# Optimization experiments

Measured on AMD Instinct MI355X. Metric: run time of the kernel, lower is better.

## Reference

```python
import jax, jax.numpy as jnp
import numpy as np
from jax import lax

B, S, IN, H, HEAD, OUT = 256, 512, 64, 1024, 128, 64


def setup_inputs() -> dict:
    key = jax.random.key(0)
    ks = jax.random.split(key, 9)
    sc = 0.05
    return {
        "x": jax.random.normal(ks[0], (B, S, IN), jnp.float32),
        "W_ih": jax.random.normal(ks[1], (4 * H, IN), jnp.float32) * sc,
        "b_ih": jax.random.normal(ks[2], (4 * H,), jnp.float32) * sc,
        "W_hh": jax.random.normal(ks[3], (4 * H, H), jnp.float32) * sc,
        "b_hh": jax.random.normal(ks[4], (4 * H,), jnp.float32) * sc,
        "W_dense": jax.random.normal(ks[5], (HEAD, H), jnp.float32) * sc,
        "b_dense": jax.random.normal(ks[6], (HEAD,), jnp.float32) * sc,
        "W_dense2": jax.random.normal(ks[7], (OUT, HEAD), jnp.float32) * sc,
        "b_dense2": jax.random.normal(ks[8], (OUT,), jnp.float32) * sc,
    }


def reference(x, W_ih, b_ih, W_hh, b_hh, W_dense, b_dense, W_dense2, b_dense2):
    batch = x.shape[0]
    hid = W_hh.shape[1]
    # Precompute input-to-gate projections for all timesteps in one big GEMM.
    # x: [B,S,IN] -> xg: [S,B,4H]
    xg = jnp.einsum("bsi,gi->sbg", x, W_ih) + b_ih + b_hh

    def step(carry, xg_t):
        h, c = carry
        gates = xg_t + h @ W_hh.T  # [B,4H]; PyTorch LSTMCell gate order i,f,g,o
        i, f, g, o = jnp.split(gates, 4, axis=-1)
        c = jax.nn.sigmoid(f) * c + jax.nn.sigmoid(i) * jnp.tanh(g)
        h = jax.nn.sigmoid(o) * jnp.tanh(c)
        pred = jax.nn.relu(h @ W_dense.T + b_dense) @ W_dense2.T + b_dense2
        return (h, c), pred

    h0 = jnp.zeros((batch, hid), x.dtype)
    c0 = jnp.zeros((batch, hid), x.dtype)
    _, out = lax.scan(step, (h0, c0), xg)  # out: [S,B,OUT]
    return jnp.swapaxes(out, 0, 1)  # [B,S,OUT]
```

## Files before the change

### kernel.cpp

```cpp
#include <hip/hip_runtime.h>

typedef _Float16 half_t;
typedef _Float16 half8 __attribute__((ext_vector_type(8)));
typedef _Float16 half4 __attribute__((ext_vector_type(4)));
typedef float float4v __attribute__((ext_vector_type(4)));

#define BB    256
#define SS    512
#define IND   64
#define HH    1024
#define HEADD 128
#define OUTD  64
#define NKT   34
#define WLDS_HALVES (4 * NKT * 512)
#define PRE_STRIDE 68
#define DP_OFF   (WLDS_HALVES * 2 + 4 * 16 * PRE_STRIDE * 4)
#define FLAG_OFF (DP_OFF + 3 * 64 * 4 * 4)
#define SMEM_BYTES (FLAG_OFF + 32)
#define BUFV (BB * HH)
#define GO_OFF   8192
#define DCNT_OFF 10240
#define SYNC_WORDS 10368

#define MFMA16(a, b, acc) __builtin_amdgcn_mfma_f32_16x16x32_f16(a, b, acc, 0, 0, 0)

__device__ half_t g_hA[(size_t)(SS + 1) * BUFV];
__device__ half_t g_dbuf[(size_t)SS * 256 * HEADD];
__device__ unsigned int g_sync[SYNC_WORDS];

__device__ __forceinline__ void astore8(half_t* p, half4 v) {
  union { half4 h; unsigned long long u; } r; r.h = v;
  __hip_atomic_store((unsigned long long*)p, r.u, __ATOMIC_RELAXED,
                     __HIP_MEMORY_SCOPE_AGENT);
}
__device__ __forceinline__ void astore2(half_t* p, half_t v) {
  union { half_t h; unsigned short u; } r; r.h = v;
  __hip_atomic_store((unsigned short*)p, r.u, __ATOMIC_RELAXED,
                     __HIP_MEMORY_SCOPE_AGENT);
}


__global__ __launch_bounds__(256) void init_state() {
  const size_t i = (size_t)blockIdx.x * 256 + threadIdx.x;
  *(unsigned long long*)(g_hA + i * 4) = 0ULL;
  if (blockIdx.x == 0)
    for (int j = threadIdx.x; j < SYNC_WORDS; j += 256) g_sync[j] = 0;
}

__global__ __launch_bounds__(256) void pack_x(const float* __restrict__ x,
                                              half_t* __restrict__ xA) {
  const int t = blockIdx.x, mt = blockIdx.y;
  const int tid = threadIdx.x;
  const int kt = tid >> 7;
  const int lane = (tid >> 1) & 63;
  const int jh = (tid & 1) * 4;
  const int row = mt * 16 + (lane & 15);
  const int k = kt * 32 + (lane >> 4) * 8 + jh;
  const float* s = x + (size_t)row * SS * IND + (size_t)t * IND + k;
  half_t* d = xA + (((size_t)t * 16 + mt) * 2 + kt) * 512 + lane * 8 + jh;
  d[0] = (half_t)s[0]; d[1] = (half_t)s[1];
  d[2] = (half_t)s[2]; d[3] = (half_t)s[3];
}

__global__ __launch_bounds__(256) void frag_pack(const float* __restrict__ src,
                                                 half_t* __restrict__ dst, int K) {
  const int cb = blockIdx.x;
  const int tid = threadIdx.x;
  const int lane = tid & 63;
  const int u = tid >> 6;
  const int nkt = K >> 5;
  const int row = cb * 16 + (lane & 15);
  for (int kt = u; kt < nkt; kt += 4) {
    const int k = kt * 32 + (lane >> 4) * 8;
    const float* s = src + (size_t)row * K + k;
    half8 h;
    #pragma unroll
    for (int j = 0; j < 8; ++j) h[j] = (half_t)s[j];
    *(half8*)(dst + ((size_t)cb * nkt + kt) * 512 + lane * 8) = h;
  }
}

__global__ __launch_bounds__(512, 2) void lstm_persistent(
    const float* __restrict__ W_hh, const float* __restrict__ W_ih,
    const float* __restrict__ b_ih, const float* __restrict__ b_hh,
    const half_t* __restrict__ xA, const half_t* __restrict__ Wd_f,
    const float* __restrict__ bd, const half_t* __restrict__ Wd2_f,
    const float* __restrict__ bd2, float* __restrict__ out) {
  extern __shared__ char smem[];
  half_t* Wlds = (half_t*)smem;
  float* pre = (float*)(smem + (size_t)WLDS_HALVES * 2);
  float* dp = (float*)(smem + DP_OFF);
  unsigned* flg = (unsigned*)(smem + FLAG_OFF);

  const int wg = blockIdx.x;
  const int mtile = wg >> 6;
  const int jtile = wg & 63;
  const int j0 = jtile * 16;
  const int tid = threadIdx.x;
  const int wave = tid >> 6;
  const int lane = tid & 63;
  const int rn = lane & 15;
  const int kq = lane >> 4;

  {
    const int g = wave & 3;
    const int row = g * HH + j0 + rn;
    for (int kt = (wave >> 2); kt < NKT; kt += 2) {
      const int k = kt * 32 + kq * 8;
      const float* s = (k < HH) ? (W_hh + (size_t)row * HH + k)
                                : (W_ih + (size_t)row * IND + (k - HH));
      half8 hv;
      #pragma unroll
      for (int j = 0; j < 8; ++j) hv[j] = (half_t)s[j];
      *(half8*)(Wlds + ((size_t)g * NKT + kt) * 512 + lane * 8) = hv;
    }
  }
  if (tid < 8) flg[tid] = 0;
  __syncthreads();

  unsigned short* slotp =
      (unsigned short*)(g_sync + ((size_t)(mtile * 64 + jtile)) * 32);
  unsigned int* go_base = g_sync + GO_OFF + mtile * 512;
  const unsigned int* gop = go_base + (jtile & 15) * 32;
  unsigned int* dcnt = g_sync + DCNT_OFF + mtile * 32;

  if (wave < 4) {
    const int crow = lane >> 2;
    const int hl = (lane & 3) * 4;
    float bsum[4][4];
    #pragma unroll
    for (int g = 0; g < 4; ++g) {
      const float4v bi = *(const float4v*)(b_ih + g * HH + j0 + hl);
      const float4v bh = *(const float4v*)(b_hh + g * HH + j0 + hl);
      #pragma unroll
      for (int j = 0; j < 4; ++j) bsum[g][j] = bi[j] + bh[j];
    }
    float4v creg = {0.f, 0.f, 0.f, 0.f};

    const int mtA = mtile * 4 + wave;
    float* pw = pre + wave * (16 * PRE_STRIDE);

    const int col_s = j0 + hl;
    const int ktw = col_s >> 5;
    const int kqw = (col_s & 31) >> 3;
    const int jw = col_s & 7;
    const size_t hoff =
        (((size_t)(mtA * 32 + ktw)) * 64 + kqw * 16 + crow) * 8 + jw;

    const half_t* habase = g_hA + ((size_t)mtA * 32) * 512 + lane * 8;
    const half_t* bp = Wlds + lane * 8;
    unsigned short* myslot = slotp + wave;

    for (int t = 0; t < SS; ++t) {
      float4v a0 = {0.f, 0.f, 0.f, 0.f}, a1 = {0.f, 0.f, 0.f, 0.f};
      float4v a2 = {0.f, 0.f, 0.f, 0.f}, a3 = {0.f, 0.f, 0.f, 0.f};

      const half_t* xp = xA + (((size_t)t * 16 + mtA) * 2) * 512 + lane * 8;
      {
        const half8 xv0 = *(const half8*)xp;
        const half8 xv1 = *(const half8*)(xp + 512);
        a0 = MFMA16(xv0, *(const half8*)(bp + (size_t)(0 * NKT + 32) * 512), a0);
        a1 = MFMA16(xv0, *(const half8*)(bp + (size_t)(1 * NKT + 32) * 512), a1);
        a2 = MFMA16(xv0, *(const half8*)(bp + (size_t)(2 * NKT + 32) * 512), a2);
        a3 = MFMA16(xv0, *(const half8*)(bp + (size_t)(3 * NKT + 32) * 512), a3);
        a0 = MFMA16(xv1, *(const half8*)(bp + (size_t)(0 * NKT + 33) * 512), a0);
        a1 = MFMA16(xv1, *(const half8*)(bp + (size_t)(1 * NKT + 33) * 512), a1);
        a2 = MFMA16(xv1, *(const half8*)(bp + (size_t)(2 * NKT + 33) * 512), a2);
        a3 = MFMA16(xv1, *(const half8*)(bp + (size_t)(3 * NKT + 33) * 512), a3);
      }

      if (t >= 1) {
        const unsigned tt = (unsigned)t;
        while (__hip_atomic_load(gop, __ATOMIC_RELAXED,
                                 __HIP_MEMORY_SCOPE_AGENT) < tt)
          __builtin_amdgcn_s_sleep(2);
        asm volatile("" ::: "memory");
        if (wave == 0 && lane == 0)
          __hip_atomic_store(&flg[3], tt, __ATOMIC_RELEASE,
                             __HIP_MEMORY_SCOPE_WORKGROUP);
      }

      const half_t* ap = habase + (size_t)t * BUFV;
      #pragma unroll 8
      for (int kt = 0; kt < 32; ++kt) {
        const half8 av = *(const half8*)(ap + (size_t)kt * 512);
        a0 = MFMA16(av, *(const half8*)(bp + (size_t)(0 * NKT + kt) * 512), a0);
        a1 = MFMA16(av, *(const half8*)(bp + (size_t)(1 * NKT + kt) * 512), a1);
        a2 = MFMA16(av, *(const half8*)(bp + (size_t)(2 * NKT + kt) * 512), a2);
        a3 = MFMA16(av, *(const half8*)(bp + (size_t)(3 * NKT + kt) * 512), a3);
      }

      #pragma unroll
      for (int r = 0; r < 4; ++r) {
        const int rl = (kq * 4 + r) * PRE_STRIDE;
        pw[rl + rn] = a0[r];
        pw[rl + 16 + rn] = a1[r];
        pw[rl + 32 + rn] = a2[r];
        pw[rl + 48 + rn] = a3[r];
      }

      const float4v pg0 = *(const float4v*)(pw + crow * PRE_STRIDE + hl);
      const float4v pg1 = *(const float4v*)(pw + crow * PRE_STRIDE + 16 + hl);
      const float4v pg2 = *(const float4v*)(pw + crow * PRE_STRIDE + 32 + hl);
      const float4v pg3 = *(const float4v*)(pw + crow * PRE_STRIDE + 48 + hl);
      half4 hnew;
      #pragma unroll
      for (int jj = 0; jj < 4; ++jj) {
        const float ig = pg0[jj] + bsum[0][jj];
        const float fg = pg1[jj] + bsum[1][jj];
        const float gg = pg2[jj] + bsum[2][jj];
        const float og = pg3[jj] + bsum[3][jj];
        const float is = 1.f / (1.f + __expf(-ig));
        const float fs = 1.f / (1.f + __expf(-fg));
        const float os = 1.f / (1.f + __expf(-og));
        const float gt = tanhf(gg);
        const float cn = fs * creg[jj] + is * gt;
        creg[jj] = cn;
        hnew[jj] = (half_t)(os * tanhf(cn));
      }
      astore8(g_hA + (size_t)(t + 1) * BUFV + hoff, hnew);

      __builtin_amdgcn_s_waitcnt(0);
      if (lane == 0)
        __hip_atomic_store(myslot, (unsigned short)(t + 1), __ATOMIC_RELAXED,
                           __HIP_MEMORY_SCOPE_AGENT);
    }

    if (wave == 0) {
      while (__hip_atomic_load(gop, __ATOMIC_RELAXED,
                               __HIP_MEMORY_SCOPE_AGENT) < (unsigned)SS)
        __builtin_amdgcn_s_sleep(2);
      asm volatile("" ::: "memory");
      if (lane == 0)
        __hip_atomic_store(&flg[3], (unsigned)SS, __ATOMIC_RELEASE,
                           __HIP_MEMORY_SCOPE_WORKGROUP);
    }

  } else if (jtile < 32) {
    const int u = wave - 4;
    const int rb = jtile >> 3, cb = jtile & 7;
    const int mt = mtile * 4 + rb;
    const half_t* hb = g_hA + ((size_t)mt * 32 + u * 8) * 512 + lane * 8;
    const half_t* bb = Wd_f + ((size_t)cb * 32 + u * 8) * 512 + lane * 8;

    for (int s = 1; s <= SS; ++s) {
      while (__hip_atomic_load(&flg[3], __ATOMIC_ACQUIRE,
                               __HIP_MEMORY_SCOPE_WORKGROUP) < (unsigned)s)
        __builtin_amdgcn_s_sleep(2);
      asm volatile("" ::: "memory");

      const half_t* ap = hb + (size_t)s * BUFV;
      float4v acc = {0.f, 0.f, 0.f, 0.f};
      #pragma unroll
      for (int kt = 0; kt < 8; ++kt)
        acc = MFMA16(*(const half8*)(ap + (size_t)kt * 512),
                     *(const half8*)(bb + (size_t)kt * 512), acc);

      if (u) {
        if (s > 1)
          while (__hip_atomic_load(&flg[4], __ATOMIC_ACQUIRE,
                                   __HIP_MEMORY_SCOPE_WORKGROUP) <
                 (unsigned)(s - 1))
            __builtin_amdgcn_s_sleep(1);
        *(float4v*)(dp + ((size_t)(u - 1) * 64 + lane) * 4) = acc;
        __hip_atomic_store(&flg[u - 1], (unsigned)s, __ATOMIC_RELEASE,
                           __HIP_MEMORY_SCOPE_WORKGROUP);
      } else {
        for (;;) {
          const unsigned f0 = __hip_atomic_load(&flg[0], __ATOMIC_ACQUIRE,
                                                __HIP_MEMORY_SCOPE_WORKGROUP);
          const unsigned f1 = __hip_atomic_load(&flg[1], __ATOMIC_ACQUIRE,
                                                __HIP_MEMORY_SCOPE_WORKGROUP);
          const unsigned f2 = __hip_atomic_load(&flg[2], __ATOMIC_ACQUIRE,
                                                __HIP_MEMORY_SCOPE_WORKGROUP);
          if (f0 >= (unsigned)s && f1 >= (unsigned)s && f2 >= (unsigned)s) break;
          __builtin_amdgcn_s_sleep(1);
        }
        asm volatile("" ::: "memory");
        #pragma unroll
        for (int i = 0; i < 3; ++i) {
          const float4v p = *(const float4v*)(dp + ((size_t)i * 64 + lane) * 4);
          #pragma unroll
          for (int r = 0; r < 4; ++r) acc[r] += p[r];
        }
        __hip_atomic_store(&flg[4], (unsigned)s, __ATOMIC_RELEASE,
                           __HIP_MEMORY_SCOPE_WORKGROUP);
        const int dcol = cb * 16 + rn;
        const float bv = bd[dcol];
        half_t* db = g_dbuf + (((size_t)(s - 1) * 16 + mt) * 16) * HEADD + dcol;
        #pragma unroll
        for (int r = 0; r < 4; ++r)
          astore2(db + (size_t)(kq * 4 + r) * HEADD,
                  (half_t)fmaxf(acc[r] + bv, 0.f));
        __builtin_amdgcn_s_waitcnt(0);
        if (lane == 0)
          __hip_atomic_fetch_add(dcnt, 1u, __ATOMIC_RELAXED,
                                 __HIP_MEMORY_SCOPE_AGENT);
      }
    }

  } else if (jtile < 48 && wave == 4) {
    const int task = jtile - 32;
    const int rb = task >> 2, cb2 = task & 3;
    const int mt = mtile * 4 + rb;
    const int m0 = mtile * 64;
    const half_t* bp2 = Wd2_f + (size_t)cb2 * 4 * 512 + lane * 8;
    for (int d = 0; d < SS; ++d) {
      if (lane == 0) {
        const unsigned tgt = 32u * (unsigned)(d + 1);
        while (__hip_atomic_load(dcnt, __ATOMIC_RELAXED,
                                 __HIP_MEMORY_SCOPE_AGENT) < tgt)
          __builtin_amdgcn_s_sleep(16);
      }
      asm volatile("" ::: "memory");
      const half_t* ap = g_dbuf + (((size_t)d * 16 + mt) * 16) * HEADD;
      float4v acc = {0.f, 0.f, 0.f, 0.f};
      #pragma unroll
      for (int kt = 0; kt < 4; ++kt) {
        const half8 af =
            *(const half8*)(ap + (size_t)rn * HEADD + kt * 32 + kq * 8);
        acc = MFMA16(af, *(const half8*)(bp2 + (size_t)kt * 512), acc);
      }
      const int ocol = cb2 * 16 + rn;
      const float bv = bd2[ocol];
      #pragma unroll
      for (int r = 0; r < 4; ++r) {
        const int row = m0 + rb * 16 + kq * 4 + r;
        out[(size_t)row * (SS * OUTD) + (size_t)d * OUTD + ocol] = acc[r] + bv;
      }
    }

  } else if (jtile == 63 && wave == 5) {
    const unsigned long long* pollp =
        (const unsigned long long*)(g_sync + ((size_t)(mtile * 64 + lane)) * 32);
    for (int t = 1; t <= SS; ++t) {
      const unsigned tt = (unsigned)t;
      for (;;) {
        const unsigned long long v = __hip_atomic_load(
            pollp, __ATOMIC_RELAXED, __HIP_MEMORY_SCOPE_AGENT);
        const unsigned f0 = (unsigned)(v & 0xffffu);
        const unsigned f1 = (unsigned)((v >> 16) & 0xffffu);
        const unsigned f2 = (unsigned)((v >> 32) & 0xffffu);
        const unsigned f3 = (unsigned)(v >> 48);
        if (__all((int)(f0 >= tt && f1 >= tt && f2 >= tt && f3 >= tt))) break;
        __builtin_amdgcn_s_sleep(2);
      }
      asm volatile("" ::: "memory");
      if (lane < 16)
        __hip_atomic_store(go_base + lane * 32, tt, __ATOMIC_RELAXED,
                           __HIP_MEMORY_SCOPE_AGENT);
    }
  }
}

extern "C" void kernel_launch(void* const* d_in, const int* in_sizes, int n_in,
                              void* d_out, int out_size, void* d_ws, size_t ws_size,
                              hipStream_t stream) {
  const float* x        = (const float*)d_in[0];
  const float* W_ih     = (const float*)d_in[1];
  const float* b_ih     = (const float*)d_in[2];
  const float* W_hh     = (const float*)d_in[3];
  const float* b_hh     = (const float*)d_in[4];
  const float* W_dense  = (const float*)d_in[5];
  const float* b_dense  = (const float*)d_in[6];
  const float* W_dense2 = (const float*)d_in[7];
  const float* b_dense2 = (const float*)d_in[8];
  float* out = (float*)d_out;

  char* p = (char*)d_ws;
  half_t* xA    = (half_t*)p; p += (size_t)SS * 16 * 1024 * 2;
  half_t* Wd_f  = (half_t*)p; p += (size_t)8 * 32 * 512 * 2;
  half_t* Wd2_f = (half_t*)p; p += (size_t)4 * 4 * 512 * 2;

  init_state<<<256, 256, 0, stream>>>();
  pack_x<<<dim3(SS, 16), 256, 0, stream>>>(x, xA);
  frag_pack<<<HEADD / 16, 256, 0, stream>>>(W_dense, Wd_f, HH);
  frag_pack<<<OUTD / 16, 256, 0, stream>>>(W_dense2, Wd2_f, HEADD);

  hipFuncSetAttribute((const void*)lstm_persistent,
                      hipFuncAttributeMaxDynamicSharedMemorySize, SMEM_BYTES);
  void* args[] = {(void*)&W_hh, (void*)&W_ih, (void*)&b_ih, (void*)&b_hh,
                  (void*)&xA, (void*)&Wd_f, (void*)&b_dense,
                  (void*)&Wd2_f, (void*)&b_dense2, (void*)&out};
  hipLaunchCooperativeKernel((void*)lstm_persistent, dim3(256), dim3(512),
                             args, SMEM_BYTES, stream);
}
```

Before: 4.797 ms.

## Replace aggregator-wave barrier with per-chunk atomic counters and staged K-waits

Drops the dedicated aggregator wave that polled every workgroup's slot flags and broadcast a go counter. Each workgroup now counts its four waves' completion in LDS and the last wave increments one of four global per-timestep chunk counters. The recurrent GEMM is split into four K-chunks, and each chunk waits only on the counter for the producers of that slice, so MFMA work can start before all of h_t is ready. This removes one hop of barrier latency from the serial timestep chain, at the cost of more global atomic contention and more polling loads.

```diff
diff --git a/kernel.cpp b/kernel.cpp
--- a/kernel.cpp
+++ b/kernel.cpp
@@ -16,11 +16,10 @@
 #define PRE_STRIDE 68
 #define DP_OFF   (WLDS_HALVES * 2 + 4 * 16 * PRE_STRIDE * 4)
 #define FLAG_OFF (DP_OFF + 3 * 64 * 4 * 4)
-#define SMEM_BYTES (FLAG_OFF + 32)
+#define SMEM_BYTES (FLAG_OFF + 96)
 #define BUFV (BB * HH)
-#define GO_OFF   8192
-#define DCNT_OFF 10240
-#define SYNC_WORDS 10368
+#define DCNT_OFF 8192
+#define SYNC_WORDS 8320
 
 #define MFMA16(a, b, acc) __builtin_amdgcn_mfma_f32_16x16x32_f16(a, b, acc, 0, 0, 0)
 
@@ -91,6 +90,7 @@
   float* pre = (float*)(smem + (size_t)WLDS_HALVES * 2);
   float* dp = (float*)(smem + DP_OFF);
   unsigned* flg = (unsigned*)(smem + FLAG_OFF);
+  unsigned* wgdone = flg + 8;
 
   const int wg = blockIdx.x;
   const int mtile = wg >> 6;
@@ -116,12 +116,10 @@
     }
   }
   if (tid < 8) flg[tid] = 0;
+  if (tid >= 8 && tid < 24) wgdone[tid - 8] = 0;
   __syncthreads();
 
-  unsigned short* slotp =
-      (unsigned short*)(g_sync + ((size_t)(mtile * 64 + jtile)) * 32);
-  unsigned int* go_base = g_sync + GO_OFF + mtile * 512;
-  const unsigned int* gop = go_base + (jtile & 15) * 32;
+  unsigned int* cbase = g_sync + (size_t)mtile * 2048;
   unsigned int* dcnt = g_sync + DCNT_OFF + mtile * 32;
 
   if (wave < 4) {
@@ -149,9 +147,21 @@
 
     const half_t* habase = g_hA + ((size_t)mtA * 32) * 512 + lane * 8;
     const half_t* bp = Wlds + lane * 8;
-    unsigned short* myslot = slotp + wave;
+    const int mychunk = jtile >> 4;
 
     for (int t = 0; t < SS; ++t) {
+      unsigned r0 = 16u, r1 = 16u, r2 = 16u, r3 = 16u;
+      if (t >= 1) {
+        r0 = __hip_atomic_load(cbase + 0 * 512 + (t - 1), __ATOMIC_RELAXED,
+                               __HIP_MEMORY_SCOPE_AGENT);
+        r1 = __hip_atomic_load(cbase + 1 * 512 + (t - 1), __ATOMIC_RELAXED,
+                               __HIP_MEMORY_SCOPE_AGENT);
+        r2 = __hip_atomic_load(cbase + 2 * 512 + (t - 1), __ATOMIC_RELAXED,
+                               __HIP_MEMORY_SCOPE_AGENT);
+        r3 = __hip_atomic_load(cbase + 3 * 512 + (t - 1), __ATOMIC_RELAXED,
+                               __HIP_MEMORY_SCOPE_AGENT);
+      }
+
       float4v a0 = {0.f, 0.f, 0.f, 0.f}, a1 = {0.f, 0.f, 0.f, 0.f};
       float4v a2 = {0.f, 0.f, 0.f, 0.f}, a3 = {0.f, 0.f, 0.f, 0.f};
 
@@ -169,25 +179,30 @@
         a3 = MFMA16(xv1, *(const half8*)(bp + (size_t)(3 * NKT + 33) * 512), a3);
       }
 
-      if (t >= 1) {
-        const unsigned tt = (unsigned)t;
-        while (__hip_atomic_load(gop, __ATOMIC_RELAXED,
-                                 __HIP_MEMORY_SCOPE_AGENT) < tt)
-          __builtin_amdgcn_s_sleep(2);
-        asm volatile("" ::: "memory");
-        if (wave == 0 && lane == 0)
-          __hip_atomic_store(&flg[3], tt, __ATOMIC_RELEASE,
-                             __HIP_MEMORY_SCOPE_WORKGROUP);
-      }
-
       const half_t* ap = habase + (size_t)t * BUFV;
-      #pragma unroll 8
-      for (int kt = 0; kt < 32; ++kt) {
-        const half8 av = *(const half8*)(ap + (size_t)kt * 512);
-        a0 = MFMA16(av, *(const half8*)(bp + (size_t)(0 * NKT + kt) * 512), a0);
-        a1 = MFMA16(av, *(const half8*)(bp + (size_t)(1 * NKT + kt) * 512), a1);
-        a2 = MFMA16(av, *(const half8*)(bp + (size_t)(2 * NKT + kt) * 512), a2);
-        a3 = MFMA16(av, *(const half8*)(bp + (size_t)(3 * NKT + kt) * 512), a3);
+      #pragma unroll
+      for (int q = 0; q < 4; ++q) {
+        if (t >= 1) {
+          unsigned v = (q == 0) ? r0 : (q == 1) ? r1 : (q == 2) ? r2 : r3;
+          while (v < 16u) {
+            __builtin_amdgcn_s_sleep(1);
+            v = __hip_atomic_load(cbase + q * 512 + (t - 1), __ATOMIC_RELAXED,
+                                  __HIP_MEMORY_SCOPE_AGENT);
+          }
+          asm volatile("" ::: "memory");
+          if (q == 3 && wave == 0 && lane == 0)
+            __hip_atomic_store(&flg[3], (unsigned)t, __ATOMIC_RELEASE,
+                               __HIP_MEMORY_SCOPE_WORKGROUP);
+        }
+        #pragma unroll
+        for (int k2 = 0; k2 < 8; ++k2) {
+          const int kt = q * 8 + k2;
+          const half8 av = *(const half8*)(ap + (size_t)kt * 512);
+          a0 = MFMA16(av, *(const half8*)(bp + (size_t)(0 * NKT + kt) * 512), a0);
+          a1 = MFMA16(av, *(const half8*)(bp + (size_t)(1 * NKT + kt) * 512), a1);
+          a2 = MFMA16(av, *(const half8*)(bp + (size_t)(2 * NKT + kt) * 512), a2);
+          a3 = MFMA16(av, *(const half8*)(bp + (size_t)(3 * NKT + kt) * 512), a3);
+        }
       }
 
       #pragma unroll
@@ -221,15 +236,24 @@
       astore8(g_hA + (size_t)(t + 1) * BUFV + hoff, hnew);
 
       __builtin_amdgcn_s_waitcnt(0);
-      if (lane == 0)
-        __hip_atomic_store(myslot, (unsigned short)(t + 1), __ATOMIC_RELAXED,
-                           __HIP_MEMORY_SCOPE_AGENT);
+      asm volatile("" ::: "memory");
+      if (lane == 0) {
+        const unsigned old = atomicAdd(&wgdone[t & 15], 1u);
+        if (old == 3u) {
+          wgdone[t & 15] = 0u;
+          __hip_atomic_fetch_add(cbase + mychunk * 512 + t, 1u,
+                                 __ATOMIC_RELAXED, __HIP_MEMORY_SCOPE_AGENT);
+        }
+      }
     }
 
     if (wave == 0) {
-      while (__hip_atomic_load(gop, __ATOMIC_RELAXED,
-                               __HIP_MEMORY_SCOPE_AGENT) < (unsigned)SS)
-        __builtin_amdgcn_s_sleep(2);
+      #pragma unroll
+      for (int q = 0; q < 4; ++q) {
+        while (__hip_atomic_load(cbase + q * 512 + (SS - 1), __ATOMIC_RELAXED,
+                                 __HIP_MEMORY_SCOPE_AGENT) < 16u)
+          __builtin_amdgcn_s_sleep(2);
+      }
       asm volatile("" ::: "memory");
       if (lane == 0)
         __hip_atomic_store(&flg[3], (unsigned)SS, __ATOMIC_RELEASE,
@@ -329,27 +353,6 @@
         out[(size_t)row * (SS * OUTD) + (size_t)d * OUTD + ocol] = acc[r] + bv;
       }
     }
-
-  } else if (jtile == 63 && wave == 5) {
-    const unsigned long long* pollp =
-        (const unsigned long long*)(g_sync + ((size_t)(mtile * 64 + lane)) * 32);
-    for (int t = 1; t <= SS; ++t) {
-      const unsigned tt = (unsigned)t;
-      for (;;) {
-        const unsigned long long v = __hip_atomic_load(
-            pollp, __ATOMIC_RELAXED, __HIP_MEMORY_SCOPE_AGENT);
-        const unsigned f0 = (unsigned)(v & 0xffffu);
-        const unsigned f1 = (unsigned)((v >> 16) & 0xffffu);
-        const unsigned f2 = (unsigned)((v >> 32) & 0xffffu);
-        const unsigned f3 = (unsigned)(v >> 48);
-        if (__all((int)(f0 >= tt && f1 >= tt && f2 >= tt && f3 >= tt))) break;
-        __builtin_amdgcn_s_sleep(2);
-      }
-      asm volatile("" ::: "memory");
-      if (lane < 16)
-        __hip_atomic_store(go_base + lane * 32, tt, __ATOMIC_RELAXED,
-                           __HIP_MEMORY_SCOPE_AGENT);
-    }
   }
 }
 
```

Measured after the change: 5.884 ms. +22.6%, slower.

## Split step barrier into per-quarter go flags so GEMM starts on partial h

Applied to the files above, without the earlier changes.

The coordinator wave now reduces completion slots per group of 16 workgroups and publishes four separate go counters (one per K-quarter of h) rather than a single all-done flag. Gate-compute waves begin the recurrent GEMM as soon as the first quarter is ready and wait for each later quarter just before its K-slice. Dense-head waves poll their own quarter's go flag directly instead of the workgroup-local relay flag. The aim is to overlap the global step barrier with MFMA work, at the cost of more polling traffic and a more complex, fragile synchronization protocol.

```diff
diff --git a/kernel.cpp b/kernel.cpp
--- a/kernel.cpp
+++ b/kernel.cpp
@@ -80,6 +80,15 @@
   }
 }
 
+#define GKT(kt)                                                               \
+  {                                                                           \
+    const half8 av = *(const half8*)(ap + (size_t)(kt) * 512);                \
+    a0 = MFMA16(av, *(const half8*)(bp + (size_t)(0 * NKT + (kt)) * 512), a0);\
+    a1 = MFMA16(av, *(const half8*)(bp + (size_t)(1 * NKT + (kt)) * 512), a1);\
+    a2 = MFMA16(av, *(const half8*)(bp + (size_t)(2 * NKT + (kt)) * 512), a2);\
+    a3 = MFMA16(av, *(const half8*)(bp + (size_t)(3 * NKT + (kt)) * 512), a3);\
+  }
+
 __global__ __launch_bounds__(512, 2) void lstm_persistent(
     const float* __restrict__ W_hh, const float* __restrict__ W_ih,
     const float* __restrict__ b_ih, const float* __restrict__ b_hh,
@@ -121,7 +130,7 @@
   unsigned short* slotp =
       (unsigned short*)(g_sync + ((size_t)(mtile * 64 + jtile)) * 32);
   unsigned int* go_base = g_sync + GO_OFF + mtile * 512;
-  const unsigned int* gop = go_base + (jtile & 15) * 32;
+  const unsigned int* goline = go_base + (jtile & 15) * 32;
   unsigned int* dcnt = g_sync + DCNT_OFF + mtile * 32;
 
   if (wave < 4) {
@@ -152,6 +161,18 @@
     unsigned short* myslot = slotp + wave;
 
     for (int t = 0; t < SS; ++t) {
+      unsigned g0 = 0, g1 = 0, g2 = 0, g3 = 0;
+      if (t >= 1) {
+        const unsigned long long v01 = __hip_atomic_load(
+            (const unsigned long long*)goline, __ATOMIC_RELAXED,
+            __HIP_MEMORY_SCOPE_AGENT);
+        const unsigned long long v23 = __hip_atomic_load(
+            (const unsigned long long*)(goline + 2), __ATOMIC_RELAXED,
+            __HIP_MEMORY_SCOPE_AGENT);
+        g0 = (unsigned)v01; g1 = (unsigned)(v01 >> 32);
+        g2 = (unsigned)v23; g3 = (unsigned)(v23 >> 32);
+      }
+
       float4v a0 = {0.f, 0.f, 0.f, 0.f}, a1 = {0.f, 0.f, 0.f, 0.f};
       float4v a2 = {0.f, 0.f, 0.f, 0.f}, a3 = {0.f, 0.f, 0.f, 0.f};
 
@@ -169,25 +190,43 @@
         a3 = MFMA16(xv1, *(const half8*)(bp + (size_t)(3 * NKT + 33) * 512), a3);
       }
 
-      if (t >= 1) {
+      const half_t* ap = habase + (size_t)t * BUFV;
+      if (t == 0) {
+        #pragma unroll 8
+        for (int kt = 0; kt < 32; ++kt) GKT(kt)
+      } else {
         const unsigned tt = (unsigned)t;
-        while (__hip_atomic_load(gop, __ATOMIC_RELAXED,
-                                 __HIP_MEMORY_SCOPE_AGENT) < tt)
+        while (g0 < tt) {
           __builtin_amdgcn_s_sleep(2);
+          const unsigned long long v01 = __hip_atomic_load(
+              (const unsigned long long*)goline, __ATOMIC_RELAXED,
+              __HIP_MEMORY_SCOPE_AGENT);
+          const unsigned long long v23 = __hip_atomic_load(
+              (const unsigned long long*)(goline + 2), __ATOMIC_RELAXED,
+              __HIP_MEMORY_SCOPE_AGENT);
+          g0 = (unsigned)v01; g1 = (unsigned)(v01 >> 32);
+          g2 = (unsigned)v23; g3 = (unsigned)(v23 >> 32);
+        }
         asm volatile("" ::: "memory");
-        if (wave == 0 && lane == 0)
-          __hip_atomic_store(&flg[3], tt, __ATOMIC_RELEASE,
-                             __HIP_MEMORY_SCOPE_WORKGROUP);
-      }
-
-      const half_t* ap = habase + (size_t)t * BUFV;
-      #pragma unroll 8
-      for (int kt = 0; kt < 32; ++kt) {
-        const half8 av = *(const half8*)(ap + (size_t)kt * 512);
-        a0 = MFMA16(av, *(const half8*)(bp + (size_t)(0 * NKT + kt) * 512), a0);
-        a1 = MFMA16(av, *(const half8*)(bp + (size_t)(1 * NKT + kt) * 512), a1);
-        a2 = MFMA16(av, *(const half8*)(bp + (size_t)(2 * NKT + kt) * 512), a2);
-        a3 = MFMA16(av, *(const half8*)(bp + (size_t)(3 * NKT + kt) * 512), a3);
+        if (g1 >= tt && g2 >= tt && g3 >= tt) {
+          #pragma unroll 8
+          for (int kt = 0; kt < 32; ++kt) GKT(kt)
+        } else {
+          #pragma unroll
+          for (int k2 = 0; k2 < 8; ++k2) GKT(k2)
+          #pragma unroll
+          for (int q = 1; q < 4; ++q) {
+            unsigned gq = (q == 1) ? g1 : (q == 2) ? g2 : g3;
+            while (gq < tt) {
+              __builtin_amdgcn_s_sleep(2);
+              gq = __hip_atomic_load(goline + q, __ATOMIC_RELAXED,
+                                     __HIP_MEMORY_SCOPE_AGENT);
+            }
+            asm volatile("" ::: "memory");
+            #pragma unroll
+            for (int k2 = 0; k2 < 8; ++k2) GKT(q * 8 + k2)
+          }
+        }
       }
 
       #pragma unroll
@@ -226,26 +265,17 @@
                            __HIP_MEMORY_SCOPE_AGENT);
     }
 
-    if (wave == 0) {
-      while (__hip_atomic_load(gop, __ATOMIC_RELAXED,
-                               __HIP_MEMORY_SCOPE_AGENT) < (unsigned)SS)
-        __builtin_amdgcn_s_sleep(2);
-      asm volatile("" ::: "memory");
-      if (lane == 0)
-        __hip_atomic_store(&flg[3], (unsigned)SS, __ATOMIC_RELEASE,
-                           __HIP_MEMORY_SCOPE_WORKGROUP);
-    }
-
   } else if (jtile < 32) {
     const int u = wave - 4;
     const int rb = jtile >> 3, cb = jtile & 7;
     const int mt = mtile * 4 + rb;
     const half_t* hb = g_hA + ((size_t)mt * 32 + u * 8) * 512 + lane * 8;
     const half_t* bb = Wd_f + ((size_t)cb * 32 + u * 8) * 512 + lane * 8;
+    const unsigned int* myg = goline + u;
 
     for (int s = 1; s <= SS; ++s) {
-      while (__hip_atomic_load(&flg[3], __ATOMIC_ACQUIRE,
-                               __HIP_MEMORY_SCOPE_WORKGROUP) < (unsigned)s)
+      while (__hip_atomic_load(myg, __ATOMIC_RELAXED,
+                               __HIP_MEMORY_SCOPE_AGENT) < (unsigned)s)
         __builtin_amdgcn_s_sleep(2);
       asm volatile("" ::: "memory");
 
@@ -333,23 +363,30 @@
   } else if (jtile == 63 && wave == 5) {
     const unsigned long long* pollp =
         (const unsigned long long*)(g_sync + ((size_t)(mtile * 64 + lane)) * 32);
-    for (int t = 1; t <= SS; ++t) {
-      const unsigned tt = (unsigned)t;
-      for (;;) {
-        const unsigned long long v = __hip_atomic_load(
-            pollp, __ATOMIC_RELAXED, __HIP_MEMORY_SCOPE_AGENT);
-        const unsigned f0 = (unsigned)(v & 0xffffu);
-        const unsigned f1 = (unsigned)((v >> 16) & 0xffffu);
-        const unsigned f2 = (unsigned)((v >> 32) & 0xffffu);
-        const unsigned f3 = (unsigned)(v >> 48);
-        if (__all((int)(f0 >= tt && f1 >= tt && f2 >= tt && f3 >= tt))) break;
-        __builtin_amdgcn_s_sleep(2);
-      }
-      asm volatile("" ::: "memory");
-      if (lane < 16)
-        __hip_atomic_store(go_base + lane * 32, tt, __ATOMIC_RELAXED,
-                           __HIP_MEMORY_SCOPE_AGENT);
-    }
+    unsigned int* myg = go_base + (lane & 15) * 32 + (lane >> 4);
+    unsigned prev = 0;
+    for (;;) {
+      const unsigned long long v = __hip_atomic_load(
+          pollp, __ATOMIC_RELAXED, __HIP_MEMORY_SCOPE_AGENT);
+      const unsigned f0 = (unsigned)(v & 0xffffu);
+      const unsigned f1 = (unsigned)((v >> 16) & 0xffffu);
+      const unsigned f2 = (unsigned)((v >> 32) & 0xffffu);
+      const unsigned f3 = (unsigned)(v >> 48);
+      unsigned m0v = f0 < f1 ? f0 : f1;
+      const unsigned m1v = f2 < f3 ? f2 : f3;
+      unsigned m = m0v < m1v ? m0v : m1v;
+      #pragma unroll
+      for (int off = 1; off < 16; off <<= 1) {
+        const unsigned o = (unsigned)__shfl_xor((int)m, off);
+        m = o < m ? o : m;
+      }
+      if (m > prev) {
+        __hip_atomic_store(myg, m, __ATOMIC_RELAXED, __HIP_MEMORY_SCOPE_AGENT);
+        prev = m;
+      }
+      if (__all((int)(m >= (unsigned)SS))) break;
+    }
+    __builtin_amdgcn_s_waitcnt(0);
   }
 }
 
```

After: 5.955 ms. 24.1% more time.
